# Kernel optimization log

Measured on AMD Instinct MI355X. Metric: run time of the kernel, lower is better.

The kernel has to match this reference:

```python
import jax, jax.numpy as jnp
import numpy as np

B, S, D, E, H = 1024, 256, 1024, 1024, 1024  # batch, state, belief, embedding, hidden
T1 = 32            # clip_length => number of scan steps
POSE_TILES = 4
MIN_STD = 0.1


def _gru(x, h, wih, whh, bih, bhh):
    # torch.nn.GRUCell semantics
    gi = x @ wih.T + bih
    gh = h @ whh.T + bhh
    i_r, i_z, i_n = jnp.split(gi, 3, axis=-1)
    h_r, h_z, h_n = jnp.split(gh, 3, axis=-1)
    r = jax.nn.sigmoid(i_r + h_r)
    z = jax.nn.sigmoid(i_z + h_z)
    n = jnp.tanh(i_n + r * h_n)
    return (1.0 - z) * n + z * h


def setup_inputs() -> dict:
    key = jax.random.key(0)
    ks = iter(jax.random.split(key, 40))
    g = lambda shape, s=1.0: jax.random.normal(next(ks), shape, dtype=jnp.float32) * s
    W = 0.02
    inp = {
        'prev_state': g((B, S)),
        'prev_belief': g((B, D)),
        'observations': g((T1, B, E)),
        'poses': g((T1, B, 6)),
        'noise_post': g((T1, B, S)),
        'noise_prior': g((T1, B, S)),
        # fc_embed_state_posterior: (2S+E) -> D
        'W_esq': g((D, 2 * S + E), W), 'b_esq': jnp.zeros((D,), jnp.float32),
        # fc_embed_state_prior: (2S+6*pose_tiles) -> D
        'W_esp': g((D, 2 * S + 6 * POSE_TILES), W), 'b_esp': jnp.zeros((D,), jnp.float32),
        # GRUCell posterior / prior
        'gq_wih': g((3 * D, D), W), 'gq_whh': g((3 * D, D), W),
        'gq_bih': jnp.zeros((3 * D,), jnp.float32), 'gq_bhh': jnp.zeros((3 * D,), jnp.float32),
        'gp_wih': g((3 * D, D), W), 'gp_whh': g((3 * D, D), W),
        'gp_bih': jnp.zeros((3 * D,), jnp.float32), 'gp_bhh': jnp.zeros((3 * D,), jnp.float32),
        # belief -> hidden -> 2*state heads
        'W_ebq': g((H, D), W), 'b_ebq': jnp.zeros((H,), jnp.float32),
        'W_sq': g((2 * S, H), W), 'b_sq': jnp.zeros((2 * S,), jnp.float32),
        'W_ebp': g((H, D), W), 'b_ebp': jnp.zeros((H,), jnp.float32),
        'W_sp': g((2 * S, H), W), 'b_sp': jnp.zeros((2 * S,), jnp.float32),
    }
    return inp


def reference(prev_state, prev_belief, observations, poses, noise_post, noise_prior,
              W_esq, b_esq, W_esp, b_esp,
              gq_wih, gq_whh, gq_bih, gq_bhh,
              gp_wih, gp_whh, gp_bih, gp_bhh,
              W_ebq, b_ebq, W_sq, b_sq, W_ebp, b_ebp, W_sp, b_sp):
    relu = jax.nn.relu

    def step(carry, xs):
        s_q, s_p, b_q, b_p = carry
        obs, pose, nq, npn = xs
        # posterior branch
        h = relu(jnp.concatenate([obs, s_q, s_p], axis=1) @ W_esq.T + b_esq)
        b_q_new = _gru(h, b_q, gq_wih, gq_whh, gq_bih, gq_bhh)
        hq = relu(b_q_new @ W_ebq.T + b_ebq)
        mq, raw_sq = jnp.split(hq @ W_sq.T + b_sq, 2, axis=1)
        std_q = jax.nn.softplus(raw_sq) + MIN_STD
        s_q_new = mq + std_q * nq
        # prior branch (uses old s_q, s_p per original code)
        pose_t = jnp.tile(pose, (1, POSE_TILES))
        h2 = relu(jnp.concatenate([pose_t, s_q, s_p], axis=1) @ W_esp.T + b_esp)
        b_p_new = _gru(h2, b_p, gp_wih, gp_whh, gp_bih, gp_bhh)
        hp = relu(b_p_new @ W_ebp.T + b_ebp)
        mp, raw_sp = jnp.split(hp @ W_sp.T + b_sp, 2, axis=1)
        std_p = jax.nn.softplus(raw_sp) + MIN_STD
        s_p_new = mp + std_p * npn
        new_carry = (s_q_new, s_p_new, b_q_new, b_p_new)
        ys = (b_q_new, s_p_new, mp, std_p, s_q_new, mq, std_q)
        return new_carry, ys

    carry0 = (prev_state, prev_state, prev_belief, prev_belief)
    _, ys = jax.lax.scan(step, carry0, (observations, poses, noise_post, noise_prior))
    post_beliefs, prior_states, prior_means, prior_stds, post_states, post_means, post_stds = ys
    # order matches torch: [posterior_beliefs, prior_states, prior_means, prior_std_devs,
    #                       posterior_states, posterior_means, posterior_std_devs]
    return (post_beliefs, prior_states, prior_means, prior_stds,
            post_states, post_means, post_stds)
```

## Files before the change

kernel.cpp:

```cpp
#include <hip/hip_runtime.h>
#include <stdint.h>
#include <math.h>

typedef unsigned short ushort_t;
typedef __attribute__((ext_vector_type(8))) short bf16x8;
typedef __attribute__((ext_vector_type(4))) float f32x4;

#define T1_ 32

__device__ __forceinline__ float bf2f(ushort_t u) {
  union { unsigned int i; float f; } v; v.i = ((unsigned int)u) << 16; return v.f;
}
__device__ __forceinline__ ushort_t f2bf(float f) {
  union { float f; unsigned int i; } v; v.f = f;
  unsigned int x = v.i;
  return (ushort_t)((x + 0x7FFFu + ((x >> 16) & 1u)) >> 16);
}
__device__ __forceinline__ float sigm(float x) { return 1.f / (1.f + expf(-x)); }

__device__ __forceinline__ void gld16(const ushort_t* g, ushort_t* l) {
  __builtin_amdgcn_global_load_lds(
      (const __attribute__((address_space(1))) unsigned int*)g,
      (__attribute__((address_space(3))) unsigned int*)l, 16, 0, 0);
}

__global__ __launch_bounds__(256) void cvt_k(const float* src, ushort_t* dst,
                                             long long n, int cols, int src_ld, int src_off) {
  const long long idx = (long long)blockIdx.x * 256 + threadIdx.x;
  if (idx >= n) return;
  const long long row = idx / cols;
  const int col = (int)(idx - row * cols);
  dst[idx] = f2bf(src[row * src_ld + src_off + col]);
}

__global__ __launch_bounds__(256) void wpe_k(const float* Wesp, float* wpe) {
  const int i = blockIdx.x * 256 + threadIdx.x;
  if (i >= 1024 * 6) return;
  const int n = i / 6, j = i % 6;
  float s = 0.f;
#pragma unroll
  for (int r = 0; r < 4; ++r) s += Wesp[(long long)n * 536 + j + 6 * r];
  wpe[i] = s;
}

__global__ void marker_k(float* out, float K) {
  if (threadIdx.x == 0 && blockIdx.x == 0) out[0] = K;
}

struct MMSide {
  const ushort_t* a0; const ushort_t* a1; const ushort_t* a2;
  int kd0, kd1, kd2;
  int coff0, coff1, coff2;
  const ushort_t* W; int ldw;
  const float* bias;
  ushort_t* outb;
  int dopose;
};
struct MM2Args { MMSide s[2]; const float* poses_t; const float* wpe; };

__global__ __launch_bounds__(256) void mm2_k(MM2Args g) {
  const MMSide S = g.s[blockIdx.z];
  __shared__ __align__(16) ushort_t As[2][2048];
  __shared__ __align__(16) ushort_t Ws[2][4096];
  const int tid = threadIdx.x;
  const int lane = tid & 63, wave = tid >> 6;
  const int wm = wave >> 1, wn = wave & 1;
  const int bn0 = blockIdx.x * 128, bm0 = blockIdx.y * 64;

  f32x4 acc[2][4];
#pragma unroll
  for (int i = 0; i < 2; ++i)
#pragma unroll
    for (int j = 0; j < 4; ++j) acc[i][j] = (f32x4){0.f, 0.f, 0.f, 0.f};

  const int rowA = tid >> 2, kcA = (tid & 3) * 8;
  const int nk0 = S.kd0 >> 5, nk1 = S.kd1 >> 5, nk2 = S.kd2 >> 5;
  const int c1 = nk0, c2 = nk0 + nk1, nkt = c2 + nk2;

  auto stage = [&](int buf, int ktg) {
    const ushort_t* ab; int ktl, kdim, cf;
    if (ktg < c1)      { ab = S.a0; ktl = ktg;      kdim = S.kd0; cf = S.coff0; }
    else if (ktg < c2) { ab = S.a1; ktl = ktg - c1; kdim = S.kd1; cf = S.coff1; }
    else               { ab = S.a2; ktl = ktg - c2; kdim = S.kd2; cf = S.coff2; }
    const int k0 = ktl * 32;
    gld16(ab + (long long)(bm0 + rowA) * kdim + k0 + kcA, &As[buf][wave * 512]);
    gld16(S.W + cf + (long long)(bn0 + rowA) * S.ldw + k0 + kcA, &Ws[buf][wave * 512]);
    gld16(S.W + cf + (long long)(bn0 + 64 + rowA) * S.ldw + k0 + kcA, &Ws[buf][2048 + wave * 512]);
  };

  stage(0, 0);
  __syncthreads();
  int cur = 0;
#pragma unroll 1
  for (int ktg = 0; ktg < nkt; ++ktg) {
    if (ktg + 1 < nkt) stage(cur ^ 1, ktg + 1);
    const int r15 = lane & 15, kh = (lane >> 4) * 8;
    bf16x8 a[2], b[4];
#pragma unroll
    for (int i = 0; i < 2; ++i)
      a[i] = *(const bf16x8*)&As[cur][(wm * 32 + i * 16 + r15) * 32 + kh];
#pragma unroll
    for (int j = 0; j < 4; ++j)
      b[j] = *(const bf16x8*)&Ws[cur][(wn * 64 + j * 16 + r15) * 32 + kh];
#pragma unroll
    for (int i = 0; i < 2; ++i)
#pragma unroll
      for (int j = 0; j < 4; ++j)
        acc[i][j] = __builtin_amdgcn_mfma_f32_16x16x32_bf16(a[i], b[j], acc[i][j], 0, 0, 0);
    __syncthreads();
    cur ^= 1;
  }

  const int r15 = lane & 15, rq = (lane >> 4) * 4;
#pragma unroll
  for (int i = 0; i < 2; ++i) {
#pragma unroll
    for (int j = 0; j < 4; ++j) {
      const int col = bn0 + wn * 64 + j * 16 + r15;
      const float bs = S.bias[col];
#pragma unroll
      for (int q = 0; q < 4; ++q) {
        const int row = bm0 + wm * 32 + i * 16 + rq + q;
        float v = acc[i][j][q] + bs;
        if (S.dopose) {
          float s = 0.f;
#pragma unroll
          for (int jj = 0; jj < 6; ++jj)
            s += g.poses_t[(long long)row * 6 + jj] * g.wpe[col * 6 + jj];
          v += s;
        }
        v = fmaxf(v, 0.f);
        S.outb[(size_t)row * 1024 + col] = f2bf(v);
      }
    }
  }
}

struct GruSide {
  const ushort_t* x;
  const ushort_t* hb;
  const float* hf;
  const ushort_t* wih; const ushort_t* whh;
  const float* bih; const float* bhh;
  float* dst; ushort_t* dstb;
};
struct Gru2Args { GruSide s[2]; };

__global__ __launch_bounds__(512) void gru2_k(Gru2Args g) {
  const GruSide S = g.s[blockIdx.z];
  __shared__ __align__(16) ushort_t Xs[2][4096];
  __shared__ __align__(16) ushort_t Hs[2][4096];
  __shared__ __align__(16) ushort_t Wt[2][6][2048];
  const int tid = threadIdx.x;
  const int lane = tid & 63, wave = tid >> 6;
  const int wm = wave >> 1, wn = wave & 1;
  const int bn0 = blockIdx.x * 64, bm0 = blockIdx.y * 128;

  f32x4 acc[6][2][2];
#pragma unroll
  for (int gg = 0; gg < 6; ++gg)
#pragma unroll
    for (int i = 0; i < 2; ++i)
#pragma unroll
      for (int j = 0; j < 2; ++j) acc[gg][i][j] = (f32x4){0.f, 0.f, 0.f, 0.f};

  const int rowA = tid >> 2, kc = (tid & 3) * 8;
  const long long xoff = (long long)(bm0 + rowA) * 1024 + kc;

  auto stage = [&](int buf, int kt) {
    const int k0 = kt * 32;
    gld16(S.x + xoff + k0, &Xs[buf][wave * 512]);
    gld16(S.hb + xoff + k0, &Hs[buf][wave * 512]);
#pragma unroll
    for (int r = 0; r < 3; ++r) {
      const int q = tid + 512 * r;
      const int gg = q >> 8;
      const int qq = q & 255;
      const int wrow = qq >> 2, wkc = (qq & 3) * 8;
      const ushort_t* base = (gg < 3) ? S.wih : S.whh;
      const int grow = (gg % 3) * 1024 + bn0 + wrow;
      gld16(base + (long long)grow * 1024 + k0 + wkc,
            &Wt[buf][0][0] + wave * 512 + r * 4096);
    }
  };

  stage(0, 0);
  __syncthreads();
  int cur = 0;
#pragma unroll 1
  for (int kt = 0; kt < 32; ++kt) {
    if (kt + 1 < 32) stage(cur ^ 1, kt + 1);
    const int r15 = lane & 15, kh = (lane >> 4) * 8;
    bf16x8 ax[2], ah[2];
#pragma unroll
    for (int i = 0; i < 2; ++i) {
      ax[i] = *(const bf16x8*)&Xs[cur][(wm * 32 + i * 16 + r15) * 32 + kh];
      ah[i] = *(const bf16x8*)&Hs[cur][(wm * 32 + i * 16 + r15) * 32 + kh];
    }
#pragma unroll
    for (int gg = 0; gg < 6; ++gg) {
      bf16x8 bw[2];
#pragma unroll
      for (int j = 0; j < 2; ++j)
        bw[j] = *(const bf16x8*)&Wt[cur][gg][(wn * 32 + j * 16 + r15) * 32 + kh];
#pragma unroll
      for (int i = 0; i < 2; ++i)
#pragma unroll
        for (int j = 0; j < 2; ++j)
          acc[gg][i][j] = __builtin_amdgcn_mfma_f32_16x16x32_bf16(
              (gg < 3) ? ax[i] : ah[i], bw[j], acc[gg][i][j], 0, 0, 0);
    }
    __syncthreads();
    cur ^= 1;
  }

  const int r15 = lane & 15, rq = (lane >> 4) * 4;
#pragma unroll
  for (int j = 0; j < 2; ++j) {
    const int col = bn0 + wn * 32 + j * 16 + r15;
    const float br  = S.bih[col],        bhr = S.bhh[col];
    const float bz  = S.bih[col + 1024], bhz = S.bhh[col + 1024];
    const float bn_ = S.bih[col + 2048], bhn = S.bhh[col + 2048];
#pragma unroll
    for (int i = 0; i < 2; ++i) {
#pragma unroll
      for (int q = 0; q < 4; ++q) {
        const int row = bm0 + wm * 32 + i * 16 + rq + q;
        const float ir = acc[0][i][j][q] + br,   hr = acc[3][i][j][q] + bhr;
        const float iz = acc[1][i][j][q] + bz,   hz = acc[4][i][j][q] + bhz;
        const float in_ = acc[2][i][j][q] + bn_, hn = acc[5][i][j][q] + bhn;
        const float r = sigm(ir + hr);
        const float z = sigm(iz + hz);
        const float ng = tanhf(in_ + r * hn);
        const long long o = (long long)row * 1024 + col;
        const float bnew = (1.f - z) * ng + z * S.hf[o];
        S.dst[o] = bnew;
        S.dstb[o] = f2bf(bnew);
      }
    }
  }
}

struct HeadSide {
  const ushort_t* hh;
  const ushort_t* Ws;
  const float* bs;
  const float* noise;
  float* omean; float* ostd; float* ostate;
  ushort_t* stateb;
};
struct Head2Args { HeadSide s[2]; };

__global__ __launch_bounds__(256) void head2_k(Head2Args g) {
  const HeadSide S = g.s[blockIdx.z];
  __shared__ __align__(16) ushort_t As[2][2048];
  __shared__ __align__(16) ushort_t Wt[2][2][2048];
  const int tid = threadIdx.x;
  const int lane = tid & 63, wave = tid >> 6;
  const int wm = wave >> 1, wn = wave & 1;
  const int bn0 = blockIdx.x * 64, bm0 = blockIdx.y * 64;

  f32x4 acc[2][2][2];
#pragma unroll
  for (int gg = 0; gg < 2; ++gg)
#pragma unroll
    for (int i = 0; i < 2; ++i)
#pragma unroll
      for (int j = 0; j < 2; ++j) acc[gg][i][j] = (f32x4){0.f, 0.f, 0.f, 0.f};

  const int rowA = tid >> 2, kc = (tid & 3) * 8;
  const long long aoff = (long long)(bm0 + rowA) * 1024 + kc;

  auto stage = [&](int buf, int kt) {
    const int k0 = kt * 32;
    gld16(S.hh + aoff + k0, &As[buf][wave * 512]);
#pragma unroll
    for (int gg = 0; gg < 2; ++gg)
      gld16(S.Ws + (long long)(gg * 256 + bn0 + rowA) * 1024 + k0 + kc,
            &Wt[buf][gg][wave * 512]);
  };

  stage(0, 0);
  __syncthreads();
  int cur = 0;
#pragma unroll 1
  for (int kt = 0; kt < 32; ++kt) {
    if (kt + 1 < 32) stage(cur ^ 1, kt + 1);
    const int r15 = lane & 15, kh = (lane >> 4) * 8;
    bf16x8 a[2];
#pragma unroll
    for (int i = 0; i < 2; ++i)
      a[i] = *(const bf16x8*)&As[cur][(wm * 32 + i * 16 + r15) * 32 + kh];
#pragma unroll
    for (int gg = 0; gg < 2; ++gg) {
      bf16x8 bw[2];
#pragma unroll
      for (int j = 0; j < 2; ++j)
        bw[j] = *(const bf16x8*)&Wt[cur][gg][(wn * 32 + j * 16 + r15) * 32 + kh];
#pragma unroll
      for (int i = 0; i < 2; ++i)
#pragma unroll
        for (int j = 0; j < 2; ++j)
          acc[gg][i][j] = __builtin_amdgcn_mfma_f32_16x16x32_bf16(a[i], bw[j], acc[gg][i][j], 0, 0, 0);
    }
    __syncthreads();
    cur ^= 1;
  }

  const int r15 = lane & 15, rq = (lane >> 4) * 4;
#pragma unroll
  for (int j = 0; j < 2; ++j) {
    const int col = bn0 + wn * 32 + j * 16 + r15;
    const float bm = S.bs[col];
    const float bsd = S.bs[col + 256];
#pragma unroll
    for (int i = 0; i < 2; ++i) {
#pragma unroll
      for (int q = 0; q < 4; ++q) {
        const int row = bm0 + wm * 32 + i * 16 + rq + q;
        const float mean = acc[0][i][j][q] + bm;
        const float rs = acc[1][i][j][q] + bsd;
        const float sp = fmaxf(rs, 0.f) + log1pf(expf(-fabsf(rs)));
        const float sd = sp + 0.1f;
        const long long o = (long long)row * 256 + col;
        const float st = mean + sd * S.noise[o];
        S.omean[o] = mean; S.ostd[o] = sd; S.ostate[o] = st;
        S.stateb[o] = f2bf(st);
      }
    }
  }
}

extern "C" void kernel_launch(void* const* d_in, const int* in_sizes, int n_in,
                              void* d_out, int out_size, void* d_ws, size_t ws_size,
                              hipStream_t stream) {
  float* out = (float*)d_out;

  int gid = 0;
  if (n_in != 26) gid = 1;
  else if (out_size != 83886080) gid = 2;
  else if (in_sizes[0] != 262144 || in_sizes[1] != 1048576 || in_sizes[2] != 33554432 ||
           in_sizes[3] != 196608 || in_sizes[4] != 8388608 || in_sizes[5] != 8388608) gid = 3;
  else if (in_sizes[6] != 1572864 || in_sizes[8] != 548864) gid = 4;
  else if (in_sizes[10] != 3145728 || in_sizes[11] != 3145728 ||
           in_sizes[14] != 3145728 || in_sizes[15] != 3145728) gid = 5;
  else if (in_sizes[18] != 1048576 || in_sizes[20] != 524288 ||
           in_sizes[22] != 1048576 || in_sizes[24] != 524288) gid = 6;
  else if (ws_size < (128ull << 20)) gid = 7;
  if (gid != 0) {
    unsigned wsMB = (unsigned)(ws_size >> 20); if (wsMB > 4095u) wsMB = 4095u;
    const float K = (float)gid * 16777216.0f + (float)wsMB;
    hipLaunchKernelGGL(marker_k, dim3(1), dim3(64), 0, stream, out, K);
    return;
  }

  const float* prev_state  = (const float*)d_in[0];
  const float* prev_belief = (const float*)d_in[1];
  const float* observations= (const float*)d_in[2];
  const float* poses       = (const float*)d_in[3];
  const float* noise_post  = (const float*)d_in[4];
  const float* noise_prior = (const float*)d_in[5];
  const float* W_esq = (const float*)d_in[6];  const float* b_esq = (const float*)d_in[7];
  const float* W_esp = (const float*)d_in[8];  const float* b_esp = (const float*)d_in[9];
  const float* gq_wih = (const float*)d_in[10]; const float* gq_whh = (const float*)d_in[11];
  const float* gq_bih = (const float*)d_in[12]; const float* gq_bhh = (const float*)d_in[13];
  const float* gp_wih = (const float*)d_in[14]; const float* gp_whh = (const float*)d_in[15];
  const float* gp_bih = (const float*)d_in[16]; const float* gp_bhh = (const float*)d_in[17];
  const float* W_ebq = (const float*)d_in[18]; const float* b_ebq = (const float*)d_in[19];
  const float* W_sq  = (const float*)d_in[20]; const float* b_sq  = (const float*)d_in[21];
  const float* W_ebp = (const float*)d_in[22]; const float* b_ebp = (const float*)d_in[23];
  const float* W_sp  = (const float*)d_in[24]; const float* b_sp  = (const float*)d_in[25];

  float* out_belief = out;
  float* out_pstate = out + 33554432LL;
  float* out_pmean  = out + 41943040LL;
  float* out_pstd   = out + 50331648LL;
  float* out_qstate = out + 58720256LL;
  float* out_qmean  = out + 67108864LL;
  float* out_qstd   = out + 75497472LL;

  char* w = (char*)d_ws;
  ushort_t* obsb  = (ushort_t*)(w);
  ushort_t* wWesq = (ushort_t*)(w + (64ull << 20));
  ushort_t* wWesp = (ushort_t*)(w + (67ull << 20));
  ushort_t* wGqih = (ushort_t*)(w + (68ull << 20));
  ushort_t* wGqhh = (ushort_t*)(w + (74ull << 20));
  ushort_t* wGpih = (ushort_t*)(w + (80ull << 20));
  ushort_t* wGphh = (ushort_t*)(w + (86ull << 20));
  ushort_t* wEbq  = (ushort_t*)(w + (92ull << 20));
  ushort_t* wEbp  = (ushort_t*)(w + (94ull << 20));
  ushort_t* wSq   = (ushort_t*)(w + (96ull << 20));
  ushort_t* wSp   = (ushort_t*)(w + (97ull << 20));
  float*    wpe   = (float*)(w + (98ull << 20));
  ushort_t* h_q   = (ushort_t*)(w + (99ull << 20));
  ushort_t* h_p   = (ushort_t*)(w + (101ull << 20));
  ushort_t* bqb[2] = { (ushort_t*)(w + (103ull << 20)), (ushort_t*)(w + (105ull << 20)) };
  ushort_t* bpb[2] = { (ushort_t*)(w + (107ull << 20)), (ushort_t*)(w + (109ull << 20)) };
  ushort_t* sqb   = (ushort_t*)(w + (111ull << 20));
  ushort_t* spb   = (ushort_t*)(w + (111ull << 20) + 524288);
  float*    bpf[2] = { (float*)(w + (112ull << 20)), (float*)(w + (116ull << 20)) };

  const dim3 blk(256);
  auto cvt = [&](const float* s, ushort_t* d, long long n, int c, int ld, int off) {
    hipLaunchKernelGGL(cvt_k, dim3((unsigned)((n + 255) / 256)), blk, 0, stream, s, d, n, c, ld, off);
  };
  cvt(observations, obsb, 33554432LL, 1024, 1024, 0);
  cvt(W_esq, wWesq, 1572864LL, 1536, 1536, 0);
  cvt(W_esp, wWesp, 524288LL, 512, 536, 24);
  cvt(gq_wih, wGqih, 3145728LL, 1024, 1024, 0);
  cvt(gq_whh, wGqhh, 3145728LL, 1024, 1024, 0);
  cvt(gp_wih, wGpih, 3145728LL, 1024, 1024, 0);
  cvt(gp_whh, wGphh, 3145728LL, 1024, 1024, 0);
  cvt(W_ebq, wEbq, 1048576LL, 1024, 1024, 0);
  cvt(W_ebp, wEbp, 1048576LL, 1024, 1024, 0);
  cvt(W_sq, wSq, 524288LL, 1024, 1024, 0);
  cvt(W_sp, wSp, 524288LL, 1024, 1024, 0);
  cvt(prev_state, sqb, 262144LL, 256, 256, 0);
  cvt(prev_state, spb, 262144LL, 256, 256, 0);
  cvt(prev_belief, bqb[1], 1048576LL, 1024, 1024, 0);
  cvt(prev_belief, bpb[1], 1048576LL, 1024, 1024, 0);
  hipLaunchKernelGGL(wpe_k, dim3(24), blk, 0, stream, W_esp, wpe);

  for (int t = 0; t < T1_; ++t) {
    const int cur = t & 1, prv = cur ^ 1;
    const ushort_t* obs_t = obsb + (long long)t * 1048576;
    const float* bq_prev_f = (t == 0) ? prev_belief : out_belief + (long long)(t - 1) * 1048576;
    const float* bp_prev_f = (t == 0) ? prev_belief : bpf[prv];

    MM2Args a{};
    a.s[0] = MMSide{ obs_t, sqb, spb, 1024, 256, 256, 0, 1024, 1280,
                     wWesq, 1536, b_esq, h_q, 0 };
    a.s[1] = MMSide{ sqb, spb, nullptr, 256, 256, 0, 0, 256, 0,
                     wWesp, 512, b_esp, h_p, 1 };
    a.poses_t = poses + (long long)t * 6144; a.wpe = wpe;
    hipLaunchKernelGGL(mm2_k, dim3(8, 16, 2), blk, 0, stream, a);

    Gru2Args gr{};
    gr.s[0] = GruSide{ h_q, bqb[prv], bq_prev_f, wGqih, wGqhh, gq_bih, gq_bhh,
                       out_belief + (long long)t * 1048576, bqb[cur] };
    gr.s[1] = GruSide{ h_p, bpb[prv], bp_prev_f, wGpih, wGphh, gp_bih, gp_bhh,
                       bpf[cur], bpb[cur] };
    hipLaunchKernelGGL(gru2_k, dim3(16, 8, 2), dim3(512), 0, stream, gr);

    a = MM2Args{};
    a.s[0] = MMSide{ bqb[cur], nullptr, nullptr, 1024, 0, 0, 0, 0, 0,
                     wEbq, 1024, b_ebq, h_q, 0 };
    a.s[1] = MMSide{ bpb[cur], nullptr, nullptr, 1024, 0, 0, 0, 0, 0,
                     wEbp, 1024, b_ebp, h_p, 0 };
    hipLaunchKernelGGL(mm2_k, dim3(8, 16, 2), blk, 0, stream, a);

    Head2Args hd{};
    hd.s[0] = HeadSide{ h_q, wSq, b_sq, noise_post + (long long)t * 262144,
                        out_qmean + (long long)t * 262144,
                        out_qstd + (long long)t * 262144,
                        out_qstate + (long long)t * 262144, sqb };
    hd.s[1] = HeadSide{ h_p, wSp, b_sp, noise_prior + (long long)t * 262144,
                        out_pmean + (long long)t * 262144,
                        out_pstd + (long long)t * 262144,
                        out_pstate + (long long)t * 262144, spb };
    hipLaunchKernelGGL(head2_k, dim3(4, 16, 2), blk, 0, stream, hd);
  }
}
```

Before: 4.035 ms.

## Use fragment-ordered LDS layout for conflict-free MFMA operand reads; merge GRU accumulators

```diff
diff --git a/kernel.cpp b/kernel.cpp
--- a/kernel.cpp
+++ b/kernel.cpp
@@ -8,9 +8,6 @@
 
 #define T1_ 32
 
-__device__ __forceinline__ float bf2f(ushort_t u) {
-  union { unsigned int i; float f; } v; v.i = ((unsigned int)u) << 16; return v.f;
-}
 __device__ __forceinline__ ushort_t f2bf(float f) {
   union { float f; unsigned int i; } v; v.f = f;
   unsigned int x = v.i;
@@ -46,6 +43,7 @@
 __global__ void marker_k(float* out, float K) {
   if (threadIdx.x == 0 && blockIdx.x == 0) out[0] = K;
 }
+
 
 struct MMSide {
   const ushort_t* a0; const ushort_t* a1; const ushort_t* a2;
@@ -63,9 +61,11 @@
   __shared__ __align__(16) ushort_t As[2][2048];
   __shared__ __align__(16) ushort_t Ws[2][4096];
   const int tid = threadIdx.x;
-  const int lane = tid & 63, wave = tid >> 6;
-  const int wm = wave >> 1, wn = wave & 1;
+  const int lane = tid & 63, wv = tid >> 6;
+  const int wm = wv >> 1, wn = wv & 1;
   const int bn0 = blockIdx.x * 128, bm0 = blockIdx.y * 64;
+  const int r16 = lane & 15, ch8 = (lane >> 4) * 8;
+  const int idx16 = (lane >> 4) * 16 + r16;
 
   f32x4 acc[2][4];
 #pragma unroll
@@ -73,7 +73,6 @@
 #pragma unroll
     for (int j = 0; j < 4; ++j) acc[i][j] = (f32x4){0.f, 0.f, 0.f, 0.f};
 
-  const int rowA = tid >> 2, kcA = (tid & 3) * 8;
   const int nk0 = S.kd0 >> 5, nk1 = S.kd1 >> 5, nk2 = S.kd2 >> 5;
   const int c1 = nk0, c2 = nk0 + nk1, nkt = c2 + nk2;
 
@@ -83,9 +82,10 @@
     else if (ktg < c2) { ab = S.a1; ktl = ktg - c1; kdim = S.kd1; cf = S.coff1; }
     else               { ab = S.a2; ktl = ktg - c2; kdim = S.kd2; cf = S.coff2; }
     const int k0 = ktl * 32;
-    gld16(ab + (long long)(bm0 + rowA) * kdim + k0 + kcA, &As[buf][wave * 512]);
-    gld16(S.W + cf + (long long)(bn0 + rowA) * S.ldw + k0 + kcA, &Ws[buf][wave * 512]);
-    gld16(S.W + cf + (long long)(bn0 + 64 + rowA) * S.ldw + k0 + kcA, &Ws[buf][2048 + wave * 512]);
+    gld16(ab + (size_t)(bm0 + wv * 16 + r16) * kdim + k0 + ch8, &As[buf][wv * 512]);
+    gld16(S.W + cf + (size_t)(bn0 + wv * 16 + r16) * S.ldw + k0 + ch8, &Ws[buf][wv * 512]);
+    gld16(S.W + cf + (size_t)(bn0 + 64 + wv * 16 + r16) * S.ldw + k0 + ch8,
+          &Ws[buf][2048 + wv * 512]);
   };
 
   stage(0, 0);
@@ -94,14 +94,13 @@
 #pragma unroll 1
   for (int ktg = 0; ktg < nkt; ++ktg) {
     if (ktg + 1 < nkt) stage(cur ^ 1, ktg + 1);
-    const int r15 = lane & 15, kh = (lane >> 4) * 8;
     bf16x8 a[2], b[4];
 #pragma unroll
     for (int i = 0; i < 2; ++i)
-      a[i] = *(const bf16x8*)&As[cur][(wm * 32 + i * 16 + r15) * 32 + kh];
+      a[i] = *(const bf16x8*)&As[cur][(wm * 2 + i) * 512 + idx16 * 8];
 #pragma unroll
     for (int j = 0; j < 4; ++j)
-      b[j] = *(const bf16x8*)&Ws[cur][(wn * 64 + j * 16 + r15) * 32 + kh];
+      b[j] = *(const bf16x8*)&Ws[cur][(wn * 4 + j) * 512 + idx16 * 8];
 #pragma unroll
     for (int i = 0; i < 2; ++i)
 #pragma unroll
@@ -148,39 +147,38 @@
 
 __global__ __launch_bounds__(512) void gru2_k(Gru2Args g) {
   const GruSide S = g.s[blockIdx.z];
-  __shared__ __align__(16) ushort_t Xs[2][4096];
-  __shared__ __align__(16) ushort_t Hs[2][4096];
-  __shared__ __align__(16) ushort_t Wt[2][6][2048];
+  __shared__ __align__(16) ushort_t lds[2][20480];
   const int tid = threadIdx.x;
-  const int lane = tid & 63, wave = tid >> 6;
-  const int wm = wave >> 1, wn = wave & 1;
+  const int lane = tid & 63, wv = tid >> 6;
+  const int wm = wv >> 1, wn = wv & 1;
   const int bn0 = blockIdx.x * 64, bm0 = blockIdx.y * 128;
-
-  f32x4 acc[6][2][2];
-#pragma unroll
-  for (int gg = 0; gg < 6; ++gg)
-#pragma unroll
-    for (int i = 0; i < 2; ++i)
-#pragma unroll
-      for (int j = 0; j < 2; ++j) acc[gg][i][j] = (f32x4){0.f, 0.f, 0.f, 0.f};
-
-  const int rowA = tid >> 2, kc = (tid & 3) * 8;
-  const long long xoff = (long long)(bm0 + rowA) * 1024 + kc;
+  const int r16 = lane & 15, ch8 = (lane >> 4) * 8;
+  const int idx16 = (lane >> 4) * 16 + r16;
+
+  f32x4 aR[2][2], aZ[2][2], aNI[2][2], aNH[2][2];
+#pragma unroll
+  for (int i = 0; i < 2; ++i)
+#pragma unroll
+    for (int j = 0; j < 2; ++j) {
+      aR[i][j] = (f32x4){0.f,0.f,0.f,0.f}; aZ[i][j] = (f32x4){0.f,0.f,0.f,0.f};
+      aNI[i][j] = (f32x4){0.f,0.f,0.f,0.f}; aNH[i][j] = (f32x4){0.f,0.f,0.f,0.f};
+    }
 
   auto stage = [&](int buf, int kt) {
     const int k0 = kt * 32;
-    gld16(S.x + xoff + k0, &Xs[buf][wave * 512]);
-    gld16(S.hb + xoff + k0, &Hs[buf][wave * 512]);
-#pragma unroll
-    for (int r = 0; r < 3; ++r) {
-      const int q = tid + 512 * r;
-      const int gg = q >> 8;
-      const int qq = q & 255;
-      const int wrow = qq >> 2, wkc = (qq & 3) * 8;
-      const ushort_t* base = (gg < 3) ? S.wih : S.whh;
-      const int grow = (gg % 3) * 1024 + bn0 + wrow;
-      gld16(base + (long long)grow * 1024 + k0 + wkc,
-            &Wt[buf][0][0] + wave * 512 + r * 4096);
+#pragma unroll
+    for (int u = 0; u < 5; ++u) {
+      const int c = wv * 5 + u;
+      if (c < 8)
+        gld16(S.x + (size_t)(bm0 + c * 16 + r16) * 1024 + k0 + ch8, &lds[buf][c * 512]);
+      else if (c < 16)
+        gld16(S.hb + (size_t)(bm0 + (c - 8) * 16 + r16) * 1024 + k0 + ch8, &lds[buf][c * 512]);
+      else {
+        const int wch = c - 16, gg = wch >> 2, rc = wch & 3;
+        const ushort_t* base = (gg < 3) ? S.wih : S.whh;
+        const int gr = (gg < 3 ? gg : gg - 3) * 1024 + bn0 + rc * 16 + r16;
+        gld16(base + (size_t)gr * 1024 + k0 + ch8, &lds[buf][8192 + gg * 2048 + rc * 512]);
+      }
     }
   };
 
@@ -190,26 +188,28 @@
 #pragma unroll 1
   for (int kt = 0; kt < 32; ++kt) {
     if (kt + 1 < 32) stage(cur ^ 1, kt + 1);
-    const int r15 = lane & 15, kh = (lane >> 4) * 8;
-    bf16x8 ax[2], ah[2];
+    bf16x8 ax[2], ah[2], w[6][2];
 #pragma unroll
     for (int i = 0; i < 2; ++i) {
-      ax[i] = *(const bf16x8*)&Xs[cur][(wm * 32 + i * 16 + r15) * 32 + kh];
-      ah[i] = *(const bf16x8*)&Hs[cur][(wm * 32 + i * 16 + r15) * 32 + kh];
-    }
-#pragma unroll
-    for (int gg = 0; gg < 6; ++gg) {
-      bf16x8 bw[2];
+      ax[i] = *(const bf16x8*)&lds[cur][(wm * 2 + i) * 512 + idx16 * 8];
+      ah[i] = *(const bf16x8*)&lds[cur][4096 + (wm * 2 + i) * 512 + idx16 * 8];
+    }
+#pragma unroll
+    for (int gg = 0; gg < 6; ++gg)
 #pragma unroll
       for (int j = 0; j < 2; ++j)
-        bw[j] = *(const bf16x8*)&Wt[cur][gg][(wn * 32 + j * 16 + r15) * 32 + kh];
-#pragma unroll
-      for (int i = 0; i < 2; ++i)
-#pragma unroll
-        for (int j = 0; j < 2; ++j)
-          acc[gg][i][j] = __builtin_amdgcn_mfma_f32_16x16x32_bf16(
-              (gg < 3) ? ax[i] : ah[i], bw[j], acc[gg][i][j], 0, 0, 0);
-    }
+        w[gg][j] = *(const bf16x8*)&lds[cur][8192 + gg * 2048 + (wn * 2 + j) * 512 + idx16 * 8];
+#pragma unroll
+    for (int i = 0; i < 2; ++i)
+#pragma unroll
+      for (int j = 0; j < 2; ++j) {
+        aR[i][j]  = __builtin_amdgcn_mfma_f32_16x16x32_bf16(ax[i], w[0][j], aR[i][j], 0, 0, 0);
+        aR[i][j]  = __builtin_amdgcn_mfma_f32_16x16x32_bf16(ah[i], w[3][j], aR[i][j], 0, 0, 0);
+        aZ[i][j]  = __builtin_amdgcn_mfma_f32_16x16x32_bf16(ax[i], w[1][j], aZ[i][j], 0, 0, 0);
+        aZ[i][j]  = __builtin_amdgcn_mfma_f32_16x16x32_bf16(ah[i], w[4][j], aZ[i][j], 0, 0, 0);
+        aNI[i][j] = __builtin_amdgcn_mfma_f32_16x16x32_bf16(ax[i], w[2][j], aNI[i][j], 0, 0, 0);
+        aNH[i][j] = __builtin_amdgcn_mfma_f32_16x16x32_bf16(ah[i], w[5][j], aNH[i][j], 0, 0, 0);
+      }
     __syncthreads();
     cur ^= 1;
   }
@@ -218,21 +218,18 @@
 #pragma unroll
   for (int j = 0; j < 2; ++j) {
     const int col = bn0 + wn * 32 + j * 16 + r15;
-    const float br  = S.bih[col],        bhr = S.bhh[col];
-    const float bz  = S.bih[col + 1024], bhz = S.bhh[col + 1024];
-    const float bn_ = S.bih[col + 2048], bhn = S.bhh[col + 2048];
+    const float brz = S.bih[col] + S.bhh[col];
+    const float bzz = S.bih[col + 1024] + S.bhh[col + 1024];
+    const float bni = S.bih[col + 2048], bnh = S.bhh[col + 2048];
 #pragma unroll
     for (int i = 0; i < 2; ++i) {
 #pragma unroll
       for (int q = 0; q < 4; ++q) {
         const int row = bm0 + wm * 32 + i * 16 + rq + q;
-        const float ir = acc[0][i][j][q] + br,   hr = acc[3][i][j][q] + bhr;
-        const float iz = acc[1][i][j][q] + bz,   hz = acc[4][i][j][q] + bhz;
-        const float in_ = acc[2][i][j][q] + bn_, hn = acc[5][i][j][q] + bhn;
-        const float r = sigm(ir + hr);
-        const float z = sigm(iz + hz);
-        const float ng = tanhf(in_ + r * hn);
-        const long long o = (long long)row * 1024 + col;
+        const float r = sigm(aR[i][j][q] + brz);
+        const float z = sigm(aZ[i][j][q] + bzz);
+        const float ng = tanhf(aNI[i][j][q] + bni + r * (aNH[i][j][q] + bnh));
+        const size_t o = (size_t)row * 1024 + col;
         const float bnew = (1.f - z) * ng + z * S.hf[o];
         S.dst[o] = bnew;
         S.dstb[o] = f2bf(bnew);
@@ -256,9 +253,11 @@
   __shared__ __align__(16) ushort_t As[2][2048];
   __shared__ __align__(16) ushort_t Wt[2][2][2048];
   const int tid = threadIdx.x;
-  const int lane = tid & 63, wave = tid >> 6;
-  const int wm = wave >> 1, wn = wave & 1;
+  const int lane = tid & 63, wv = tid >> 6;
+  const int wm = wv >> 1, wn = wv & 1;
   const int bn0 = blockIdx.x * 64, bm0 = blockIdx.y * 64;
+  const int r16 = lane & 15, ch8 = (lane >> 4) * 8;
+  const int idx16 = (lane >> 4) * 16 + r16;
 
   f32x4 acc[2][2][2];
 #pragma unroll
@@ -267,17 +266,12 @@
     for (int i = 0; i < 2; ++i)
 #pragma unroll
       for (int j = 0; j < 2; ++j) acc[gg][i][j] = (f32x4){0.f, 0.f, 0.f, 0.f};
-
-  const int rowA = tid >> 2, kc = (tid & 3) * 8;
-  const long long aoff = (long long)(bm0 + rowA) * 1024 + kc;
 
   auto stage = [&](int buf, int kt) {
     const int k0 = kt * 32;
-    gld16(S.hh + aoff + k0, &As[buf][wave * 512]);
-#pragma unroll
-    for (int gg = 0; gg < 2; ++gg)
-      gld16(S.Ws + (long long)(gg * 256 + bn0 + rowA) * 1024 + k0 + kc,
-            &Wt[buf][gg][wave * 512]);
+    gld16(S.hh + (size_t)(bm0 + wv * 16 + r16) * 1024 + k0 + ch8, &As[buf][wv * 512]);
+    gld16(S.Ws + (size_t)(bn0 + wv * 16 + r16) * 1024 + k0 + ch8, &Wt[buf][0][wv * 512]);
+    gld16(S.Ws + (size_t)(256 + bn0 + wv * 16 + r16) * 1024 + k0 + ch8, &Wt[buf][1][wv * 512]);
   };
 
   stage(0, 0);
@@ -286,17 +280,16 @@
 #pragma unroll 1
   for (int kt = 0; kt < 32; ++kt) {
     if (kt + 1 < 32) stage(cur ^ 1, kt + 1);
-    const int r15 = lane & 15, kh = (lane >> 4) * 8;
     bf16x8 a[2];
 #pragma unroll
     for (int i = 0; i < 2; ++i)
-      a[i] = *(const bf16x8*)&As[cur][(wm * 32 + i * 16 + r15) * 32 + kh];
+      a[i] = *(const bf16x8*)&As[cur][(wm * 2 + i) * 512 + idx16 * 8];
 #pragma unroll
     for (int gg = 0; gg < 2; ++gg) {
       bf16x8 bw[2];
 #pragma unroll
       for (int j = 0; j < 2; ++j)
-        bw[j] = *(const bf16x8*)&Wt[cur][gg][(wn * 32 + j * 16 + r15) * 32 + kh];
+        bw[j] = *(const bf16x8*)&Wt[cur][gg][(wn * 2 + j) * 512 + idx16 * 8];
 #pragma unroll
       for (int i = 0; i < 2; ++i)
 #pragma unroll
```

After: 4.947 ms. +22.6%, slower.
